# Performance work log

Hardware: AMD Instinct MI355X
Metric: run time of the kernel (lower is better)

Reference implementation:

```python
import jax, jax.numpy as jnp
import numpy as np

V = 100001; H = 64; E = 768; S = 200; B = 256; NB = 2; NH = 2; HD = H // NH

def ln(x, g, b, eps):
    m = x.mean(-1, keepdims=True)
    v = ((x - m) ** 2).mean(-1, keepdims=True)
    return (x - m) / jnp.sqrt(v + eps) * g + b

def setup_inputs():
    key = jax.random.key(0)
    ks = jax.random.split(key, 32)
    f = lambda i, shape: (0.02 * jax.random.normal(ks[i], shape)).astype(jnp.float32)
    inp = {}
    inp['targetSeq'] = jax.random.randint(ks[0], (B, S), 0, V)
    inp['pos'] = jax.random.randint(ks[1], (B, S), 0, V)
    inp['neg'] = jax.random.randint(ks[2], (B, S), 0, V)
    inp['review_emb'] = f(3, (V, E))
    inp['meta_emb'] = f(4, (V, E))
    inp['item_emb'] = f(5, (V, H))
    inp['pos_emb_table'] = f(6, (S, H))
    inp['featW'] = f(7, (E, H))
    inp['featb'] = jnp.zeros((H,), jnp.float32)
    inp['revln_g'] = jnp.ones((H,), jnp.float32)
    inp['revln_b'] = jnp.zeros((H,), jnp.float32)
    for j, n in enumerate(['Wq', 'Wk', 'Wv', 'Wpq', 'Wpk', 'Wfq', 'Wfk', 'Wo', 'W1', 'W2']):
        inp[n] = f(8 + j, (NB, H, H))
    for n in ['bq', 'bk', 'bv', 'bpq', 'bpk', 'bfq', 'bfk', 'bo', 'b1', 'b2']:
        inp[n] = jnp.zeros((NB, H), jnp.float32)
    inp['attn_ln_g'] = jnp.ones((NB, H), jnp.float32)
    inp['attn_ln_b'] = jnp.zeros((NB, H), jnp.float32)
    inp['fwd_ln_g'] = jnp.ones((NB, H), jnp.float32)
    inp['fwd_ln_b'] = jnp.zeros((NB, H), jnp.float32)
    inp['lastln_g'] = jnp.ones((H,), jnp.float32)
    inp['lastln_b'] = jnp.zeros((H,), jnp.float32)
    return inp

def reference(targetSeq, pos, neg, review_emb, meta_emb, item_emb, pos_emb_table, featW, featb, revln_g, revln_b, Wq, Wk, Wv, Wpq, Wpk, Wfq, Wfk, Wo, W1, W2, bq, bk, bv, bpq, bpk, bfq, bfk, bo, b1, b2, attn_ln_g, attn_ln_b, fwd_ln_g, fwd_ln_b, lastln_g, lastln_b):
    Bv, Sv = targetSeq.shape
    keep = (targetSeq != 0).astype(jnp.float32)[..., None]  # [B,S,1] timeline mask
    # feat_emb: fused review+meta features -> linear -> LayerNorm (eps=1e-5)
    feat = ln((review_emb[targetSeq] + meta_emb[targetSeq]) @ featW + featb, revln_g, revln_b, 1e-5)
    pe = jnp.broadcast_to(pos_emb_table[None, :Sv], (Bv, Sv, H))
    q = item_emb[targetSeq] * keep
    causal = jnp.where(jnp.tril(jnp.ones((Sv, Sv), bool)), 0.0, -jnp.inf).astype(jnp.float32)
    scale = 1.0 / jnp.sqrt(jnp.float32(HD))
    heads = lambda x: x.reshape(Bv, Sv, NH, HD)
    for i in range(NB):
        Qn = ln(q, attn_ln_g[i], attn_ln_b[i], 1e-8)
        qh = heads(Qn @ Wq[i] + bq[i])
        kh = heads(q @ Wk[i] + bk[i])
        vh = heads(q @ Wv[i] + bv[i])
        pq = heads(pe @ Wpq[i] + bpq[i]); pk = heads(pe @ Wpk[i] + bpk[i])
        fq = heads(feat @ Wfq[i] + bfq[i]); fk = heads(feat @ Wfk[i] + bfk[i])
        # decoupled (DIF) attention: item + position + feature score terms
        scores = (jnp.einsum('bqhd,bkhd->bhqk', qh, kh)
                  + jnp.einsum('bqhd,bkhd->bhqk', pq, pk)
                  + jnp.einsum('bqhd,bkhd->bhqk', fq, fk)) * scale + causal
        probs = jax.nn.softmax(scores, axis=-1)
        ctx = jnp.einsum('bhqk,bkhd->bqhd', probs, vh).reshape(Bv, Sv, H)
        q = ctx @ Wo[i] + bo[i] + Qn  # residual with pre-LN branch
        q = ln(q, fwd_ln_g[i], fwd_ln_b[i], 1e-8)
        q = jax.nn.relu(q @ W1[i] + b1[i]) @ W2[i] + b2[i] + q  # 1x1-conv FFN + residual
        q = q * keep
    log_feats = ln(q, lastln_g, lastln_b, 1e-8)
    pos_logits = jnp.sum(log_feats * item_emb[pos], axis=-1)
    neg_logits = jnp.sum(log_feats * item_emb[neg], axis=-1)
    return (pos_logits, neg_logits)
```

## Files before the change

### kernel.cpp

```cpp
#include <hip/hip_runtime.h>

#define DEV __device__ __forceinline__

typedef __attribute__((ext_vector_type(4))) float f32x4;
typedef __attribute__((ext_vector_type(8))) __bf16 bf16x8;

static constexpr int Bc = 256;
static constexpr int Sc = 200;
static constexpr int Hc = 64;
static constexpr int Ec = 768;
static constexpr int HDc = 32;
static constexpr int NROWS = Bc * Sc;

DEV __bf16 f2bf(float f) {
    unsigned u = __builtin_bit_cast(unsigned, f);
    unsigned short s = (unsigned short)((u + 0x7fffu + ((u >> 16) & 1u)) >> 16);
    return __builtin_bit_cast(__bf16, s);
}
DEV float bf2f(__bf16 h) {
    unsigned short s = __builtin_bit_cast(unsigned short, h);
    unsigned u = ((unsigned)s) << 16;
    return __builtin_bit_cast(float, u);
}
DEV bf16x8 ld8(const __bf16* p) { return *(const bf16x8*)p; }

DEV bf16x8 cvt8(const float* __restrict__ p) {
    f32x4 a = *(const f32x4*)p;
    f32x4 b = *(const f32x4*)(p + 4);
    bf16x8 r;
    r[0] = f2bf(a[0]); r[1] = f2bf(a[1]); r[2] = f2bf(a[2]); r[3] = f2bf(a[3]);
    r[4] = f2bf(b[0]); r[5] = f2bf(b[1]); r[6] = f2bf(b[2]); r[7] = f2bf(b[3]);
    return r;
}

DEV void gemm64(bf16x8 A0, bf16x8 A1, const __bf16* __restrict__ W,
                const float* __restrict__ bias, __bf16* __restrict__ Y,
                int m0, int ln, int quad, int maxrow)
{
#pragma unroll
    for (int nt = 0; nt < 4; nt++) {
        int col = nt * 16 + ln;
        bf16x8 w0 = ld8(W + col * 64 + quad * 8);
        bf16x8 w1 = ld8(W + col * 64 + 32 + quad * 8);
        f32x4 acc = (f32x4){0.f, 0.f, 0.f, 0.f};
        acc = __builtin_amdgcn_mfma_f32_16x16x32_bf16(A0, w0, acc, 0, 0, 0);
        acc = __builtin_amdgcn_mfma_f32_16x16x32_bf16(A1, w1, acc, 0, 0, 0);
        float bv = bias[col];
#pragma unroll
        for (int reg = 0; reg < 4; reg++) {
            int r = m0 + quad * 4 + reg;
            if (r < maxrow) Y[(long)r * 64 + col] = f2bf(acc[reg] + bv);
        }
    }
}

__global__ __launch_bounds__(256) void wconv_kernel(
    const float* __restrict__ featW,
    const float* __restrict__ Wq, const float* __restrict__ Wk, const float* __restrict__ Wv,
    const float* __restrict__ Wpq, const float* __restrict__ Wpk,
    const float* __restrict__ Wfq, const float* __restrict__ Wfk,
    const float* __restrict__ Wo, const float* __restrict__ W1, const float* __restrict__ W2,
    __bf16* __restrict__ featWt, __bf16* __restrict__ Wt)
{
    int gid = blockIdx.x * 256 + threadIdx.x;
    if (gid < Ec * Hc) {
        int k = gid >> 6, n = gid & 63;
        featWt[n * Ec + k] = f2bf(featW[gid]);
        return;
    }
    int e2 = gid - Ec * Hc;
    int mat = e2 >> 13, r = e2 & 8191, l = r >> 12, e = r & 4095, k = e >> 6, n = e & 63;
    const float* Ws[10] = {Wq, Wk, Wv, Wpq, Wpk, Wfq, Wfk, Wo, W1, W2};
    Wt[mat * 8192 + l * 4096 + n * 64 + k] = f2bf(Ws[mat][l * 4096 + e]);
}

__global__ __launch_bounds__(256) void feat_kernel(
    const int* __restrict__ tseq, const float* __restrict__ rev,
    const float* __restrict__ meta, const __bf16* __restrict__ featWt,
    const float* __restrict__ featb, const float* __restrict__ g,
    const float* __restrict__ bb, __bf16* __restrict__ out)
{
    int lane = threadIdx.x & 63, wv = threadIdx.x >> 6;
    int ln = lane & 15, quad = lane >> 4;
    int m0 = blockIdx.x * 64 + wv * 16;
    long t = tseq[m0 + ln];
    const float* rp = rev + t * Ec + quad * 8;
    const float* mp = meta + t * Ec + quad * 8;

    f32x4 acc[4];
#pragma unroll
    for (int nt = 0; nt < 4; nt++) acc[nt] = (f32x4){0.f, 0.f, 0.f, 0.f};

    for (int ks = 0; ks < Ec / 32; ks++) {
        f32x4 ra = *(const f32x4*)(rp + ks * 32);
        f32x4 rb = *(const f32x4*)(rp + ks * 32 + 4);
        f32x4 ma = *(const f32x4*)(mp + ks * 32);
        f32x4 mb = *(const f32x4*)(mp + ks * 32 + 4);
        bf16x8 a;
        a[0] = f2bf(ra[0] + ma[0]); a[1] = f2bf(ra[1] + ma[1]);
        a[2] = f2bf(ra[2] + ma[2]); a[3] = f2bf(ra[3] + ma[3]);
        a[4] = f2bf(rb[0] + mb[0]); a[5] = f2bf(rb[1] + mb[1]);
        a[6] = f2bf(rb[2] + mb[2]); a[7] = f2bf(rb[3] + mb[3]);
#pragma unroll
        for (int nt = 0; nt < 4; nt++) {
            bf16x8 bf = ld8(featWt + (nt * 16 + ln) * Ec + ks * 32 + quad * 8);
            acc[nt] = __builtin_amdgcn_mfma_f32_16x16x32_bf16(a, bf, acc[nt], 0, 0, 0);
        }
    }
#pragma unroll
    for (int reg = 0; reg < 4; reg++) {
        float vals[4]; float s = 0.f, s2 = 0.f;
#pragma unroll
        for (int nt = 0; nt < 4; nt++) {
            float v = acc[nt][reg] + featb[nt * 16 + ln];
            vals[nt] = v; s += v; s2 += v * v;
        }
#pragma unroll
        for (int m = 1; m <= 8; m <<= 1) { s += __shfl_xor(s, m, 64); s2 += __shfl_xor(s2, m, 64); }
        float mean = s * (1.f / 64.f);
        float var = s2 * (1.f / 64.f) - mean * mean;
        float inv = rsqrtf(var + 1e-5f);
        int r = m0 + quad * 4 + reg;
#pragma unroll
        for (int nt = 0; nt < 4; nt++) {
            int c = nt * 16 + ln;
            out[(long)r * Hc + c] = f2bf((vals[nt] - mean) * inv * g[c] + bb[c]);
        }
    }
}

__global__ __launch_bounds__(256) void qinit_kernel(
    const int* __restrict__ tseq, const float* __restrict__ item, __bf16* __restrict__ q)
{
    int gid = blockIdx.x * 256 + threadIdx.x;
    int r = gid >> 3, c = (gid & 7) * 8;
    long t = tseq[r];
    f32x4 v0 = *(const f32x4*)(item + t * Hc + c);
    f32x4 v1 = *(const f32x4*)(item + t * Hc + c + 4);
    float k = (t != 0) ? 1.f : 0.f;
    bf16x8 o;
    o[0] = f2bf(v0[0] * k); o[1] = f2bf(v0[1] * k); o[2] = f2bf(v0[2] * k); o[3] = f2bf(v0[3] * k);
    o[4] = f2bf(v1[0] * k); o[5] = f2bf(v1[1] * k); o[6] = f2bf(v1[2] * k); o[7] = f2bf(v1[3] * k);
    *(bf16x8*)(q + (long)r * Hc + c) = o;
}

__global__ __launch_bounds__(256) void pe_kernel(
    const float* __restrict__ pe, const __bf16* __restrict__ Wt,
    const float* __restrict__ bpq, const float* __restrict__ bpk,
    __bf16* __restrict__ pqp, __bf16* __restrict__ pkp)
{
    int l = blockIdx.x >> 2, rb = blockIdx.x & 3;
    int lane = threadIdx.x & 63, wv = threadIdx.x >> 6;
    int ln = lane & 15, quad = lane >> 4;
    int m0 = rb * 64 + wv * 16;
    int arow = m0 + ln; if (arow > Sc - 1) arow = Sc - 1;
    bf16x8 a0 = cvt8(pe + arow * Hc + quad * 8);
    bf16x8 a1 = cvt8(pe + arow * Hc + 32 + quad * 8);
    gemm64(a0, a1, Wt + 3 * 8192 + l * 4096, bpq + l * 64, pqp + l * Sc * Hc, m0, ln, quad, Sc);
    gemm64(a0, a1, Wt + 4 * 8192 + l * 4096, bpk + l * 64, pkp + l * Sc * Hc, m0, ln, quad, Sc);
}

__global__ __launch_bounds__(256) void qkvf_kernel(
    const __bf16* __restrict__ q, const __bf16* __restrict__ feat,
    const __bf16* __restrict__ Wt, int layer,
    const float* __restrict__ bq, const float* __restrict__ bk, const float* __restrict__ bv,
    const float* __restrict__ bfq, const float* __restrict__ bfk,
    const float* __restrict__ ag, const float* __restrict__ ab,
    __bf16* __restrict__ Qn, __bf16* __restrict__ qp, __bf16* __restrict__ kp,
    __bf16* __restrict__ vp, __bf16* __restrict__ fqp, __bf16* __restrict__ fkp)
{
    int lane = threadIdx.x & 63, wv = threadIdx.x >> 6;
    int ln = lane & 15, quad = lane >> 4;
    int m0 = blockIdx.x * 64 + wv * 16;
    long row = m0 + ln;
    bf16x8 aq0 = ld8(q + row * 64 + quad * 8);
    bf16x8 aq1 = ld8(q + row * 64 + 32 + quad * 8);
    bf16x8 af0 = ld8(feat + row * 64 + quad * 8);
    bf16x8 af1 = ld8(feat + row * 64 + 32 + quad * 8);

    float s = 0.f, s2 = 0.f;
#pragma unroll
    for (int j = 0; j < 8; j++) {
        float v = bf2f(aq0[j]); s += v; s2 += v * v;
        v = bf2f(aq1[j]); s += v; s2 += v * v;
    }
    s += __shfl_xor(s, 16, 64); s += __shfl_xor(s, 32, 64);
    s2 += __shfl_xor(s2, 16, 64); s2 += __shfl_xor(s2, 32, 64);
    float mean = s * (1.f / 64.f);
    float inv = rsqrtf(s2 * (1.f / 64.f) - mean * mean + 1e-8f);
    const float* agl = ag + layer * 64; const float* abl = ab + layer * 64;
    bf16x8 nq0, nq1;
#pragma unroll
    for (int j = 0; j < 8; j++) {
        int k0 = quad * 8 + j, k1 = 32 + quad * 8 + j;
        nq0[j] = f2bf((bf2f(aq0[j]) - mean) * inv * agl[k0] + abl[k0]);
        nq1[j] = f2bf((bf2f(aq1[j]) - mean) * inv * agl[k1] + abl[k1]);
    }
    *(bf16x8*)(Qn + row * 64 + quad * 8) = nq0;
    *(bf16x8*)(Qn + row * 64 + 32 + quad * 8) = nq1;

    gemm64(nq0, nq1, Wt + 0 * 8192 + layer * 4096, bq + layer * 64, qp, m0, ln, quad, NROWS);
    gemm64(aq0, aq1, Wt + 1 * 8192 + layer * 4096, bk + layer * 64, kp, m0, ln, quad, NROWS);
    gemm64(aq0, aq1, Wt + 2 * 8192 + layer * 4096, bv + layer * 64, vp, m0, ln, quad, NROWS);
    gemm64(af0, af1, Wt + 5 * 8192 + layer * 4096, bfq + layer * 64, fqp, m0, ln, quad, NROWS);
    gemm64(af0, af1, Wt + 6 * 8192 + layer * 4096, bfk + layer * 64, fkp, m0, ln, quad, NROWS);
}

__global__ __launch_bounds__(256) void attn_kernel(
    const __bf16* __restrict__ qp, const __bf16* __restrict__ kp, const __bf16* __restrict__ vp,
    const __bf16* __restrict__ pqp, const __bf16* __restrict__ pkp,
    const __bf16* __restrict__ fqp, const __bf16* __restrict__ fkp,
    __bf16* __restrict__ ctx)
{
    __shared__ float Sm[16 * 208];
    __shared__ __bf16 Vt[32 * 224];

    int bb = blockIdx.x >> 1, h = blockIdx.x & 1;
    int tid = threadIdx.x;
    int lane = tid & 63, wv = tid >> 6;
    int ln = lane & 15, quad = lane >> 4;
    const int hc = h * HDc;
    const long base = (long)bb * Sc;
    const float scale = 0.17677669529663687f;
    __bf16* P = (__bf16*)Sm;

    for (int idx = tid; idx < Sc * HDc; idx += 256) {
        int k = idx >> 5, n = idx & 31;
        Vt[n * 224 + k] = vp[(base + k) * Hc + hc + n];
    }
    for (int idx = tid; idx < HDc * 24; idx += 256) {
        int n = idx / 24, k = 200 + idx % 24;
        Vt[n * 224 + k] = __builtin_bit_cast(__bf16, (unsigned short)0);
    }

    for (int t = 0; t < 13; t++) {
        __syncthreads();
        int arow = t * 16 + ln; if (arow > Sc - 1) arow = Sc - 1;
        bf16x8 aq0 = ld8(qp + (base + arow) * Hc + hc + quad * 8);
        bf16x8 aq1 = ld8(pqp + (long)arow * Hc + hc + quad * 8);
        bf16x8 aq2 = ld8(fqp + (base + arow) * Hc + hc + quad * 8);
        for (int nt = wv; nt <= t; nt += 4) {
            int key = nt * 16 + ln; if (key > Sc - 1) key = Sc - 1;
            f32x4 acc = (f32x4){0.f, 0.f, 0.f, 0.f};
            acc = __builtin_amdgcn_mfma_f32_16x16x32_bf16(aq0, ld8(kp + (base + key) * Hc + hc + quad * 8), acc, 0, 0, 0);
            acc = __builtin_amdgcn_mfma_f32_16x16x32_bf16(aq1, ld8(pkp + (long)key * Hc + hc + quad * 8), acc, 0, 0, 0);
            acc = __builtin_amdgcn_mfma_f32_16x16x32_bf16(aq2, ld8(fkp + (base + key) * Hc + hc + quad * 8), acc, 0, 0, 0);
#pragma unroll
            for (int reg = 0; reg < 4; reg++)
                Sm[(quad * 4 + reg) * 208 + nt * 16 + ln] = acc[reg] * scale;
        }
        __syncthreads();
        for (int ri = 0; ri < 4; ri++) {
            int r = wv * 4 + ri;
            int qrow = t * 16 + r;
            float sv[4]; float mx = -1e30f;
#pragma unroll
            for (int j = 0; j < 4; j++) {
                int k = lane + 64 * j;
                sv[j] = (k <= qrow && k < 208) ? Sm[r * 208 + k] : -1e30f;
                mx = fmaxf(mx, sv[j]);
            }
#pragma unroll
            for (int m = 1; m <= 32; m <<= 1) mx = fmaxf(mx, __shfl_xor(mx, m, 64));
            float sum = 0.f; float pv[4];
#pragma unroll
            for (int j = 0; j < 4; j++) {
                float e = (sv[j] > -1e29f) ? __expf(sv[j] - mx) : 0.f;
                pv[j] = e; sum += e;
            }
#pragma unroll
            for (int m = 1; m <= 32; m <<= 1) sum += __shfl_xor(sum, m, 64);
            float inv = 1.f / sum;
#pragma unroll
            for (int j = 0; j < 4; j++) {
                int k = lane + 64 * j;
                if (k < 224) P[r * 416 + k] = f2bf(pv[j] * inv);
            }
        }
        __syncthreads();
        if (wv < 2) {
            int ksteps = (t + 2) >> 1;
            f32x4 acc = (f32x4){0.f, 0.f, 0.f, 0.f};
            const char* Pb = (const char*)Sm;
            for (int ks = 0; ks < ksteps; ks++) {
                bf16x8 pa = *(const bf16x8*)(Pb + ln * 832 + ks * 64 + quad * 16);
                bf16x8 vb = *(const bf16x8*)(&Vt[(wv * 16 + ln) * 224 + ks * 32 + quad * 8]);
                acc = __builtin_amdgcn_mfma_f32_16x16x32_bf16(pa, vb, acc, 0, 0, 0);
            }
#pragma unroll
            for (int reg = 0; reg < 4; reg++) {
                int r = t * 16 + quad * 4 + reg;
                if (r < Sc) ctx[(base + r) * Hc + hc + wv * 16 + ln] = f2bf(acc[reg]);
            }
        }
    }
}

__global__ __launch_bounds__(256) void ffn_kernel(
    const __bf16* __restrict__ ctx, const __bf16* __restrict__ Qn,
    const __bf16* __restrict__ WtO, const __bf16* __restrict__ Wt1, const __bf16* __restrict__ Wt2,
    const float* __restrict__ bo, const float* __restrict__ b1, const float* __restrict__ b2,
    const float* __restrict__ fg, const float* __restrict__ fb,
    const int* __restrict__ tseq, __bf16* __restrict__ qout)
{
    __shared__ __bf16 T1[4][16 * 64];
    __shared__ __bf16 T2[4][16 * 64];
    int lane = threadIdx.x & 63, wv = threadIdx.x >> 6;
    int ln = lane & 15, quad = lane >> 4;
    int m0 = blockIdx.x * 64 + wv * 16;

    bf16x8 ac0 = ld8(ctx + (long)(m0 + ln) * 64 + quad * 8);
    bf16x8 ac1 = ld8(ctx + (long)(m0 + ln) * 64 + 32 + quad * 8);

    float tv[16];
#pragma unroll
    for (int nt = 0; nt < 4; nt++) {
        int col = nt * 16 + ln;
        bf16x8 w0 = ld8(WtO + col * 64 + quad * 8);
        bf16x8 w1 = ld8(WtO + col * 64 + 32 + quad * 8);
        f32x4 acc = (f32x4){0.f, 0.f, 0.f, 0.f};
        acc = __builtin_amdgcn_mfma_f32_16x16x32_bf16(ac0, w0, acc, 0, 0, 0);
        acc = __builtin_amdgcn_mfma_f32_16x16x32_bf16(ac1, w1, acc, 0, 0, 0);
        float bov = bo[col];
#pragma unroll
        for (int reg = 0; reg < 4; reg++)
            tv[nt * 4 + reg] = acc[reg] + bov + bf2f(Qn[(long)(m0 + quad * 4 + reg) * 64 + col]);
    }
    float s[4] = {0, 0, 0, 0}, s2[4] = {0, 0, 0, 0};
#pragma unroll
    for (int reg = 0; reg < 4; reg++)
#pragma unroll
        for (int nt = 0; nt < 4; nt++) { float v = tv[nt * 4 + reg]; s[reg] += v; s2[reg] += v * v; }
#pragma unroll
    for (int m = 1; m <= 8; m <<= 1)
#pragma unroll
        for (int reg = 0; reg < 4; reg++) { s[reg] += __shfl_xor(s[reg], m, 64); s2[reg] += __shfl_xor(s2[reg], m, 64); }
    float uv[16];
#pragma unroll
    for (int reg = 0; reg < 4; reg++) {
        float mean = s[reg] * (1.f / 64.f);
        float inv = rsqrtf(s2[reg] * (1.f / 64.f) - mean * mean + 1e-8f);
#pragma unroll
        for (int nt = 0; nt < 4; nt++) {
            int col = nt * 16 + ln;
            float u = (tv[nt * 4 + reg] - mean) * inv * fg[col] + fb[col];
            uv[nt * 4 + reg] = u;
            T1[wv][(quad * 4 + reg) * 64 + col] = f2bf(u);
        }
    }
    __syncthreads();
    bf16x8 au0 = ld8(&T1[wv][ln * 64 + quad * 8]);
    bf16x8 au1 = ld8(&T1[wv][ln * 64 + 32 + quad * 8]);
#pragma unroll
    for (int nt = 0; nt < 4; nt++) {
        int col = nt * 16 + ln;
        bf16x8 w0 = ld8(Wt1 + col * 64 + quad * 8);
        bf16x8 w1 = ld8(Wt1 + col * 64 + 32 + quad * 8);
        f32x4 acc = (f32x4){0.f, 0.f, 0.f, 0.f};
        acc = __builtin_amdgcn_mfma_f32_16x16x32_bf16(au0, w0, acc, 0, 0, 0);
        acc = __builtin_amdgcn_mfma_f32_16x16x32_bf16(au1, w1, acc, 0, 0, 0);
        float b1v = b1[col];
#pragma unroll
        for (int reg = 0; reg < 4; reg++)
            T2[wv][(quad * 4 + reg) * 64 + col] = f2bf(fmaxf(acc[reg] + b1v, 0.f));
    }
    __syncthreads();
    bf16x8 ah0 = ld8(&T2[wv][ln * 64 + quad * 8]);
    bf16x8 ah1 = ld8(&T2[wv][ln * 64 + 32 + quad * 8]);
#pragma unroll
    for (int nt = 0; nt < 4; nt++) {
        int col = nt * 16 + ln;
        bf16x8 w0 = ld8(Wt2 + col * 64 + quad * 8);
        bf16x8 w1 = ld8(Wt2 + col * 64 + 32 + quad * 8);
        f32x4 acc = (f32x4){0.f, 0.f, 0.f, 0.f};
        acc = __builtin_amdgcn_mfma_f32_16x16x32_bf16(ah0, w0, acc, 0, 0, 0);
        acc = __builtin_amdgcn_mfma_f32_16x16x32_bf16(ah1, w1, acc, 0, 0, 0);
        float b2v = b2[col];
#pragma unroll
        for (int reg = 0; reg < 4; reg++) {
            int r = m0 + quad * 4 + reg;
            float v = acc[reg] + b2v + uv[nt * 4 + reg];
            v *= (tseq[r] != 0) ? 1.f : 0.f;
            qout[(long)r * 64 + col] = f2bf(v);
        }
    }
}

__global__ __launch_bounds__(256) void logits_kernel(
    const __bf16* __restrict__ q, const int* __restrict__ pos, const int* __restrict__ neg,
    const float* __restrict__ item, const float* __restrict__ lg, const float* __restrict__ lb,
    float* __restrict__ out)
{
    int row = blockIdx.x * 4 + (threadIdx.x >> 6);
    int lane = threadIdx.x & 63;
    float v = bf2f(q[(long)row * Hc + lane]);
    float s = v, s2 = v * v;
#pragma unroll
    for (int m = 1; m <= 32; m <<= 1) { s += __shfl_xor(s, m, 64); s2 += __shfl_xor(s2, m, 64); }
    float mean = s * (1.f / 64.f);
    float inv = rsqrtf(s2 * (1.f / 64.f) - mean * mean + 1e-8f);
    float lf = (v - mean) * inv * lg[lane] + lb[lane];
    long p = pos[row], n = neg[row];
    float dp = lf * item[p * Hc + lane];
    float dn = lf * item[n * Hc + lane];
#pragma unroll
    for (int m = 1; m <= 32; m <<= 1) { dp += __shfl_xor(dp, m, 64); dn += __shfl_xor(dn, m, 64); }
    if (lane == 0) { out[row] = dp; out[NROWS + row] = dn; }
}

extern "C" void kernel_launch(void* const* d_in, const int* in_sizes, int n_in,
                              void* d_out, int out_size, void* d_ws, size_t ws_size,
                              hipStream_t stream)
{
    const int* tseq = (const int*)d_in[0];
    const int* pos  = (const int*)d_in[1];
    const int* neg  = (const int*)d_in[2];
    const float* rev   = (const float*)d_in[3];
    const float* meta  = (const float*)d_in[4];
    const float* item  = (const float*)d_in[5];
    const float* pe    = (const float*)d_in[6];
    const float* featW = (const float*)d_in[7];
    const float* featb = (const float*)d_in[8];
    const float* rg    = (const float*)d_in[9];
    const float* rb    = (const float*)d_in[10];
    const float* Wq = (const float*)d_in[11]; const float* Wk = (const float*)d_in[12];
    const float* Wv = (const float*)d_in[13]; const float* Wpq = (const float*)d_in[14];
    const float* Wpk = (const float*)d_in[15]; const float* Wfq = (const float*)d_in[16];
    const float* Wfk = (const float*)d_in[17]; const float* Wo = (const float*)d_in[18];
    const float* W1 = (const float*)d_in[19]; const float* W2 = (const float*)d_in[20];
    const float* bq = (const float*)d_in[21]; const float* bk = (const float*)d_in[22];
    const float* bv = (const float*)d_in[23]; const float* bpq = (const float*)d_in[24];
    const float* bpk = (const float*)d_in[25]; const float* bfq = (const float*)d_in[26];
    const float* bfk = (const float*)d_in[27]; const float* bo = (const float*)d_in[28];
    const float* b1 = (const float*)d_in[29]; const float* b2 = (const float*)d_in[30];
    const float* ag = (const float*)d_in[31]; const float* ab = (const float*)d_in[32];
    const float* fg = (const float*)d_in[33]; const float* fb = (const float*)d_in[34];
    const float* lg = (const float*)d_in[35]; const float* lb = (const float*)d_in[36];
    float* out = (float*)d_out;

    __bf16* wsb = (__bf16*)d_ws;
    const size_t F = (size_t)NROWS * Hc;
    __bf16* feat = wsb;
    __bf16* q    = wsb + 1 * F;
    __bf16* Qn   = wsb + 2 * F;
    __bf16* qp   = wsb + 3 * F;
    __bf16* kp   = wsb + 4 * F;
    __bf16* vp   = wsb + 5 * F;
    __bf16* fqp  = wsb + 6 * F;
    __bf16* fkp  = wsb + 7 * F;
    __bf16* pqp  = wsb + 8 * F;
    __bf16* pkp  = pqp + 2 * Sc * Hc;
    __bf16* featWt = pkp + 2 * Sc * Hc;
    __bf16* Wt     = featWt + Ec * Hc;

    const int PB = NROWS / 64;
    const int LB = NROWS / 4;

    wconv_kernel<<<512, 256, 0, stream>>>(featW, Wq, Wk, Wv, Wpq, Wpk, Wfq, Wfk, Wo, W1, W2,
                                          featWt, Wt);
    qinit_kernel<<<NROWS * Hc / 8 / 256, 256, 0, stream>>>(tseq, item, q);
    feat_kernel<<<PB, 256, 0, stream>>>(tseq, rev, meta, featWt, featb, rg, rb, feat);
    pe_kernel<<<8, 256, 0, stream>>>(pe, Wt, bpq, bpk, pqp, pkp);

    for (int i = 0; i < 2; i++) {
        qkvf_kernel<<<PB, 256, 0, stream>>>(q, feat, Wt, i,
                                            bq, bk, bv, bfq, bfk, ag, ab,
                                            Qn, qp, kp, vp, fqp, fkp);
        attn_kernel<<<Bc * 2, 256, 0, stream>>>(qp, kp, vp,
                                                pqp + i * Sc * Hc, pkp + i * Sc * Hc,
                                                fqp, fkp, qp);
        ffn_kernel<<<PB, 256, 0, stream>>>(qp, Qn,
                                           Wt + 7 * 8192 + i * 4096,
                                           Wt + 8 * 8192 + i * 4096,
                                           Wt + 9 * 8192 + i * 4096,
                                           bo + i * 64, b1 + i * 64, b2 + i * 64,
                                           fg + i * 64, fb + i * 64, tseq, q);
    }
    logits_kernel<<<LB, 256, 0, stream>>>(q, pos, neg, item, lg, lb, out);
}
```

Before: 888.1 us.

## Split causal attention across balanced query-tile pairs and fuse qinit into feat kernel

The attention kernel gains a second grid dimension of 7. Each block handles a pair of query tiles (c and 12-c) so the causal work per block is balanced, and it only stages the V rows those tiles can see. The q initialisation is folded into the feature GEMM kernel, which also software-pipelines its global loads of the review/meta rows and weight fragments one k-step ahead. A readfirstlane hint makes the weight-matrix selection in the conversion kernel uniform across the wave. The cost is redundant K/V staging across the 7 blocks per batch-head and higher register pressure in the pipelined feature loop.

```diff
diff --git a/kernel.cpp b/kernel.cpp
--- a/kernel.cpp
+++ b/kernel.cpp
@@ -69,21 +69,41 @@
         return;
     }
     int e2 = gid - Ec * Hc;
-    int mat = e2 >> 13, r = e2 & 8191, l = r >> 12, e = r & 4095, k = e >> 6, n = e & 63;
+    int mat = __builtin_amdgcn_readfirstlane(e2 >> 13);
+    int r = e2 & 8191, l = r >> 12, e = r & 4095, k = e >> 6, n = e & 63;
     const float* Ws[10] = {Wq, Wk, Wv, Wpq, Wpk, Wfq, Wfk, Wo, W1, W2};
-    Wt[mat * 8192 + l * 4096 + n * 64 + k] = f2bf(Ws[mat][l * 4096 + e]);
+    const float* W = Ws[mat];
+    Wt[mat * 8192 + l * 4096 + n * 64 + k] = f2bf(W[l * 4096 + e]);
 }
 
 __global__ __launch_bounds__(256) void feat_kernel(
     const int* __restrict__ tseq, const float* __restrict__ rev,
     const float* __restrict__ meta, const __bf16* __restrict__ featWt,
     const float* __restrict__ featb, const float* __restrict__ g,
-    const float* __restrict__ bb, __bf16* __restrict__ out)
+    const float* __restrict__ bb, const float* __restrict__ item,
+    __bf16* __restrict__ out, __bf16* __restrict__ qout)
 {
     int lane = threadIdx.x & 63, wv = threadIdx.x >> 6;
     int ln = lane & 15, quad = lane >> 4;
     int m0 = blockIdx.x * 64 + wv * 16;
     long t = tseq[m0 + ln];
+
+    {
+        const float* ip = item + t * Hc + quad * 16;
+        f32x4 v0 = *(const f32x4*)ip;
+        f32x4 v1 = *(const f32x4*)(ip + 4);
+        f32x4 v2 = *(const f32x4*)(ip + 8);
+        f32x4 v3 = *(const f32x4*)(ip + 12);
+        float kf = (t != 0) ? 1.f : 0.f;
+        bf16x8 o0, o1;
+        o0[0] = f2bf(v0[0] * kf); o0[1] = f2bf(v0[1] * kf); o0[2] = f2bf(v0[2] * kf); o0[3] = f2bf(v0[3] * kf);
+        o0[4] = f2bf(v1[0] * kf); o0[5] = f2bf(v1[1] * kf); o0[6] = f2bf(v1[2] * kf); o0[7] = f2bf(v1[3] * kf);
+        o1[0] = f2bf(v2[0] * kf); o1[1] = f2bf(v2[1] * kf); o1[2] = f2bf(v2[2] * kf); o1[3] = f2bf(v2[3] * kf);
+        o1[4] = f2bf(v3[0] * kf); o1[5] = f2bf(v3[1] * kf); o1[6] = f2bf(v3[2] * kf); o1[7] = f2bf(v3[3] * kf);
+        *(bf16x8*)(qout + (long)(m0 + ln) * Hc + quad * 16) = o0;
+        *(bf16x8*)(qout + (long)(m0 + ln) * Hc + quad * 16 + 8) = o1;
+    }
+
     const float* rp = rev + t * Ec + quad * 8;
     const float* mp = meta + t * Ec + quad * 8;
 
@@ -91,21 +111,39 @@
 #pragma unroll
     for (int nt = 0; nt < 4; nt++) acc[nt] = (f32x4){0.f, 0.f, 0.f, 0.f};
 
+    f32x4 ra = *(const f32x4*)rp;
+    f32x4 rb = *(const f32x4*)(rp + 4);
+    f32x4 ma = *(const f32x4*)mp;
+    f32x4 mb = *(const f32x4*)(mp + 4);
+    bf16x8 bw[4];
+#pragma unroll
+    for (int nt = 0; nt < 4; nt++) bw[nt] = ld8(featWt + (nt * 16 + ln) * Ec + quad * 8);
+
     for (int ks = 0; ks < Ec / 32; ks++) {
-        f32x4 ra = *(const f32x4*)(rp + ks * 32);
-        f32x4 rb = *(const f32x4*)(rp + ks * 32 + 4);
-        f32x4 ma = *(const f32x4*)(mp + ks * 32);
-        f32x4 mb = *(const f32x4*)(mp + ks * 32 + 4);
+        f32x4 nra = ra, nrb = rb, nma = ma, nmb = mb;
+        bf16x8 nbw[4];
+#pragma unroll
+        for (int nt = 0; nt < 4; nt++) nbw[nt] = bw[nt];
+        if (ks < Ec / 32 - 1) {
+            nra = *(const f32x4*)(rp + (ks + 1) * 32);
+            nrb = *(const f32x4*)(rp + (ks + 1) * 32 + 4);
+            nma = *(const f32x4*)(mp + (ks + 1) * 32);
+            nmb = *(const f32x4*)(mp + (ks + 1) * 32 + 4);
+#pragma unroll
+            for (int nt = 0; nt < 4; nt++)
+                nbw[nt] = ld8(featWt + (nt * 16 + ln) * Ec + (ks + 1) * 32 + quad * 8);
+        }
         bf16x8 a;
         a[0] = f2bf(ra[0] + ma[0]); a[1] = f2bf(ra[1] + ma[1]);
         a[2] = f2bf(ra[2] + ma[2]); a[3] = f2bf(ra[3] + ma[3]);
         a[4] = f2bf(rb[0] + mb[0]); a[5] = f2bf(rb[1] + mb[1]);
         a[6] = f2bf(rb[2] + mb[2]); a[7] = f2bf(rb[3] + mb[3]);
 #pragma unroll
-        for (int nt = 0; nt < 4; nt++) {
-            bf16x8 bf = ld8(featWt + (nt * 16 + ln) * Ec + ks * 32 + quad * 8);
-            acc[nt] = __builtin_amdgcn_mfma_f32_16x16x32_bf16(a, bf, acc[nt], 0, 0, 0);
-        }
+        for (int nt = 0; nt < 4; nt++)
+            acc[nt] = __builtin_amdgcn_mfma_f32_16x16x32_bf16(a, bw[nt], acc[nt], 0, 0, 0);
+        ra = nra; rb = nrb; ma = nma; mb = nmb;
+#pragma unroll
+        for (int nt = 0; nt < 4; nt++) bw[nt] = nbw[nt];
     }
 #pragma unroll
     for (int reg = 0; reg < 4; reg++) {
@@ -127,21 +165,6 @@
             out[(long)r * Hc + c] = f2bf((vals[nt] - mean) * inv * g[c] + bb[c]);
         }
     }
-}
-
-__global__ __launch_bounds__(256) void qinit_kernel(
-    const int* __restrict__ tseq, const float* __restrict__ item, __bf16* __restrict__ q)
-{
-    int gid = blockIdx.x * 256 + threadIdx.x;
-    int r = gid >> 3, c = (gid & 7) * 8;
-    long t = tseq[r];
-    f32x4 v0 = *(const f32x4*)(item + t * Hc + c);
-    f32x4 v1 = *(const f32x4*)(item + t * Hc + c + 4);
-    float k = (t != 0) ? 1.f : 0.f;
-    bf16x8 o;
-    o[0] = f2bf(v0[0] * k); o[1] = f2bf(v0[1] * k); o[2] = f2bf(v0[2] * k); o[3] = f2bf(v0[3] * k);
-    o[4] = f2bf(v1[0] * k); o[5] = f2bf(v1[1] * k); o[6] = f2bf(v1[2] * k); o[7] = f2bf(v1[3] * k);
-    *(bf16x8*)(q + (long)r * Hc + c) = o;
 }
 
 __global__ __launch_bounds__(256) void pe_kernel(
@@ -216,6 +239,7 @@
     __shared__ __bf16 Vt[32 * 224];
 
     int bb = blockIdx.x >> 1, h = blockIdx.x & 1;
+    int c = blockIdx.y;
     int tid = threadIdx.x;
     int lane = tid & 63, wv = tid >> 6;
     int ln = lane & 15, quad = lane >> 4;
@@ -224,16 +248,20 @@
     const float scale = 0.17677669529663687f;
     __bf16* P = (__bf16*)Sm;
 
-    for (int idx = tid; idx < Sc * HDc; idx += 256) {
+    int tmax = 12 - c;
+    int KV = tmax * 16 + 16; if (KV > Sc) KV = Sc;
+    for (int idx = tid; idx < KV * 32; idx += 256) {
         int k = idx >> 5, n = idx & 31;
         Vt[n * 224 + k] = vp[(base + k) * Hc + hc + n];
     }
-    for (int idx = tid; idx < HDc * 24; idx += 256) {
-        int n = idx / 24, k = 200 + idx % 24;
+    for (int idx = tid; idx < (224 - KV) * 32; idx += 256) {
+        int k = KV + (idx >> 5), n = idx & 31;
         Vt[n * 224 + k] = __builtin_bit_cast(__bf16, (unsigned short)0);
     }
 
-    for (int t = 0; t < 13; t++) {
+    int nstep = (c == 6) ? 1 : 2;
+    for (int step = 0; step < nstep; step++) {
+        int t = step ? tmax : c;
         __syncthreads();
         int arow = t * 16 + ln; if (arow > Sc - 1) arow = Sc - 1;
         bf16x8 aq0 = ld8(qp + (base + arow) * Hc + hc + quad * 8);
@@ -458,17 +486,16 @@
 
     wconv_kernel<<<512, 256, 0, stream>>>(featW, Wq, Wk, Wv, Wpq, Wpk, Wfq, Wfk, Wo, W1, W2,
                                           featWt, Wt);
-    qinit_kernel<<<NROWS * Hc / 8 / 256, 256, 0, stream>>>(tseq, item, q);
-    feat_kernel<<<PB, 256, 0, stream>>>(tseq, rev, meta, featWt, featb, rg, rb, feat);
+    feat_kernel<<<PB, 256, 0, stream>>>(tseq, rev, meta, featWt, featb, rg, rb, item, feat, q);
     pe_kernel<<<8, 256, 0, stream>>>(pe, Wt, bpq, bpk, pqp, pkp);
 
     for (int i = 0; i < 2; i++) {
         qkvf_kernel<<<PB, 256, 0, stream>>>(q, feat, Wt, i,
                                             bq, bk, bv, bfq, bfk, ag, ab,
                                             Qn, qp, kp, vp, fqp, fkp);
-        attn_kernel<<<Bc * 2, 256, 0, stream>>>(qp, kp, vp,
-                                                pqp + i * Sc * Hc, pkp + i * Sc * Hc,
-                                                fqp, fkp, qp);
+        attn_kernel<<<dim3(Bc * 2, 7), 256, 0, stream>>>(qp, kp, vp,
+                                                         pqp + i * Sc * Hc, pkp + i * Sc * Hc,
+                                                         fqp, fkp, qp);
         ffn_kernel<<<PB, 256, 0, stream>>>(qp, Qn,
                                            Wt + 7 * 8192 + i * 4096,
                                            Wt + 8 * 8192 + i * 4096,
```

Measured after the change: 866.7 us. -2.4%, faster.
